# Optimization experiments

Hardware: AMD Instinct MI355X
Metric: run time of the kernel (lower is better)

## Reference

```python
import jax, jax.numpy as jnp
import numpy as np

B, T, D, H = 64, 512, 512, 512


def lstm_scan(x_btd, Wk, Wr, b):
    """Run an LSTM over time. x_btd: [B,T,D]. Returns (h_seq [B,T,H], h_last, c_last).
    Keras gate order: i, f, c(g), o."""
    Bsz = x_btd.shape[0]
    Hn = Wr.shape[0]
    # Precompute input projections for all timesteps in one GEMM: [B,T,4H]
    xz = jnp.einsum('btd,dg->btg', x_btd, Wk) + b

    def step(carry, xz_t):
        h, c = carry
        z = xz_t + h @ Wr  # [B,4H]
        i, f, g, o = jnp.split(z, 4, axis=-1)
        i = jax.nn.sigmoid(i)
        f = jax.nn.sigmoid(f)
        g = jnp.tanh(g)
        o = jax.nn.sigmoid(o)
        c = f * c + i * g
        h = o * jnp.tanh(c)
        return (h, c), h

    h0 = jnp.zeros((Bsz, Hn), dtype=x_btd.dtype)
    c0 = jnp.zeros((Bsz, Hn), dtype=x_btd.dtype)
    (h_last, c_last), h_seq = jax.lax.scan(step, (h0, c0), jnp.swapaxes(xz, 0, 1))
    return jnp.swapaxes(h_seq, 0, 1), h_last, c_last


def setup_inputs() -> dict:
    key = jax.random.key(0)
    ks = jax.random.split(key, 6)
    s_in = 1.0 / np.sqrt(D)
    s_h = 1.0 / np.sqrt(H)
    return {
        'x': jax.random.normal(ks[0], (B, T, D), dtype=jnp.float32),
        'Wf_k': jax.random.normal(ks[1], (D, 4 * H), dtype=jnp.float32) * s_in,
        'Wf_r': jax.random.normal(ks[2], (H, 4 * H), dtype=jnp.float32) * s_h,
        'bf': jnp.zeros((4 * H,), dtype=jnp.float32),
        'Wb_k': jax.random.normal(ks[3], (D, 4 * H), dtype=jnp.float32) * s_in,
        'Wb_r': jax.random.normal(ks[4], (H, 4 * H), dtype=jnp.float32) * s_h,
        'bb': jnp.zeros((4 * H,), dtype=jnp.float32),
    }


def reference(x, Wf_k, Wf_r, bf, Wb_k, Wb_r, bb):
    # Forward direction
    h_fwd_seq, h_fwd, _c_fwd = lstm_scan(x, Wf_k, Wf_r, bf)
    # Backward direction: run on time-reversed input, then flip outputs back
    x_rev = jnp.flip(x, axis=1)
    h_bwd_seq_rev, h_bwd, _c_bwd = lstm_scan(x_rev, Wb_k, Wb_r, bb)
    h_bwd_seq = jnp.flip(h_bwd_seq_rev, axis=1)
    # Bidirectional merge_mode='concat'
    word_emb = jnp.concatenate([h_fwd_seq, h_bwd_seq], axis=-1)  # [B,T,2H]
    sent_emb = jnp.concatenate([h_fwd, h_bwd], axis=-1)          # [B,2H]
    return (word_emb, sent_emb)
```

## Files before the change

### kernel.cpp

```cpp
#include <hip/hip_runtime.h>
#include <hip/hip_bf16.h>
#include <cstdint>
#include <cstddef>

#define Bsz 64
#define Tn  512
#define Dn  512
#define Hn  512
#define NG  2048
#define GWG 32
#define NCOL 16

typedef __attribute__((ext_vector_type(8))) short short8;
typedef __attribute__((ext_vector_type(4))) float f32x4;

union FragU { uint32_t u[4]; short8 s; };

__device__ __forceinline__ unsigned short f2bf(float f) {
  union { float f; uint32_t u; } v; v.f = f;
  uint32_t u = v.u;
  uint32_t r = (u + 0x7fffu + ((u >> 16) & 1u)) >> 16;
  return (unsigned short)r;
}

__device__ __forceinline__ float sigm(float x) { return 1.0f / (1.0f + __expf(-x)); }
__device__ __forceinline__ float tanh_f(float x) { return 1.0f - 2.0f / (__expf(2.0f * x) + 1.0f); }

__global__ __launch_bounds__(256) void cast_x_kernel(const float* __restrict__ x,
                                                     unsigned short* __restrict__ xb) {
  size_t i = ((size_t)blockIdx.x * 256 + threadIdx.x) * 8;
  f32x4 a = *(const f32x4*)(x + i);
  f32x4 b = *(const f32x4*)(x + i + 4);
  short8 r;
  r[0] = (short)f2bf(a[0]); r[1] = (short)f2bf(a[1]);
  r[2] = (short)f2bf(a[2]); r[3] = (short)f2bf(a[3]);
  r[4] = (short)f2bf(b[0]); r[5] = (short)f2bf(b[1]);
  r[6] = (short)f2bf(b[2]); r[7] = (short)f2bf(b[3]);
  *(short8*)(xb + i) = r;
}

__global__ __launch_bounds__(256) void swizzle_w_kernel(
    const float* __restrict__ Wfk, const float* __restrict__ Wfr,
    const float* __restrict__ Wbk, const float* __restrict__ Wbr,
    unsigned short* __restrict__ wkf, unsigned short* __restrict__ wrf)
{
  int idx = blockIdx.x * 256 + threadIdx.x;
  int arr  = blockIdx.y;
  int lane = idx & 63;
  int kc   = (idx >> 6) & 15;
  int nt   = (idx >> 10) & 3;
  int wg   = (idx >> 12) & 31;
  int dir  = (idx >> 17) & 1;
  const float* W = arr ? (dir ? Wbr : Wfr) : (dir ? Wbk : Wfk);
  unsigned short* dst = (arr ? wrf : wkf) + (size_t)idx * 8;
  int n  = nt * 512 + wg * NCOL + (lane & 15);
  int k0 = kc * 32 + ((lane >> 4) & 3) * 8;
#pragma unroll
  for (int j = 0; j < 8; ++j) dst[j] = f2bf(W[(size_t)(k0 + j) * NG + n]);
}

__global__ __launch_bounds__(256, 1) void lstm_main_kernel(
    const unsigned short* __restrict__ xb,
    const unsigned short* __restrict__ wkf,
    const unsigned short* __restrict__ wrf,
    const float* __restrict__ bias_f, const float* __restrict__ bias_b,
    unsigned short* __restrict__ hbuf,
    int* __restrict__ flags,
    float* __restrict__ out)
{
  const int wg   = blockIdx.x;
  const int dir  = blockIdx.y;
  const int tid  = threadIdx.x;
  const int lane = tid & 63;
  const int wv   = tid >> 6;
  const int quad = lane >> 4;
  const int col  = lane & 15;

  __shared__ short8 wr_lds[4 * 16 * 64];

  {
    const short8* src = (const short8*)wrf + (size_t)(dir * GWG + wg) * 4096;
    for (int i = tid; i < 4096; i += 256) wr_lds[i] = src[i];
  }
  const short8* wk = (const short8*)wkf + (size_t)(dir * GWG + wg) * 4096;

  const float* bias = dir ? bias_b : bias_f;
  float bz[4];
#pragma unroll
  for (int g = 0; g < 4; ++g) bz[g] = bias[g * 512 + wg * NCOL + col];

  float cst[4] = {0.f, 0.f, 0.f, 0.f};

  const int am = wv * 16 + col;
  unsigned short* hf_base = hbuf + (size_t)dir * 65536;
  int* flgbase = flags + dir * Tn * 4 * GWG;

  const int kcW = wg >> 1;
  const int c0  = col & ~1;
  const int qd2 = (((wg & 1) << 4) + c0) >> 3;
  const int j2  = c0 & 7;
  const int r0  = (col & 1) << 1;
  const int eBase = (((wv * 16 + kcW) * 64 + qd2 * 16 + quad * 4 + r0) * 8 + j2) >> 1;

  __syncthreads();

  for (int t = 0; t < Tn; ++t) {
    const int tx = dir ? (Tn - 1 - t) : t;
    f32x4 a0 = {0.f,0.f,0.f,0.f}, a1 = {0.f,0.f,0.f,0.f};
    f32x4 a2 = {0.f,0.f,0.f,0.f}, a3 = {0.f,0.f,0.f,0.f};

    const short8* xrow = (const short8*)(xb + ((size_t)am * Tn + tx) * Dn);
#pragma unroll 4
    for (int kc = 0; kc < 16; ++kc) {
      short8 a = xrow[kc * 4 + quad];
      a0 = __builtin_amdgcn_mfma_f32_16x16x32_bf16(a, wk[(0*16+kc)*64 + lane], a0, 0,0,0);
      a1 = __builtin_amdgcn_mfma_f32_16x16x32_bf16(a, wk[(1*16+kc)*64 + lane], a1, 0,0,0);
      a2 = __builtin_amdgcn_mfma_f32_16x16x32_bf16(a, wk[(2*16+kc)*64 + lane], a2, 0,0,0);
      a3 = __builtin_amdgcn_mfma_f32_16x16x32_bf16(a, wk[(3*16+kc)*64 + lane], a3, 0,0,0);
    }

    if (t > 0) {
      const int* fl = flgbase + ((t - 1) * 4 + wv) * GWG;
      for (;;) {
        int v = __hip_atomic_load(fl + (lane & 31), __ATOMIC_RELAXED, __HIP_MEMORY_SCOPE_AGENT);
        if (__ballot(v != 0) == ~0ull) break;
        __builtin_amdgcn_s_sleep(1);
      }
    }

    const uint32_t* hp = (const uint32_t*)(hf_base + ((t & 1) ^ 1) * 32768);
    uint32_t*       hc = (uint32_t*)(hf_base + (t & 1) * 32768);

    FragU hfr[16];
#pragma unroll
    for (int kc = 0; kc < 16; ++kc) {
      const uint32_t* p = hp + ((size_t)(wv * 16 + kc) * 64 + lane) * 4;
#pragma unroll
      for (int d = 0; d < 4; ++d)
        hfr[kc].u[d] = __hip_atomic_load(p + d, __ATOMIC_RELAXED, __HIP_MEMORY_SCOPE_AGENT);
    }

#pragma unroll
    for (int kc = 0; kc < 16; ++kc) {
      short8 a = hfr[kc].s;
      a0 = __builtin_amdgcn_mfma_f32_16x16x32_bf16(a, wr_lds[(0*16+kc)*64 + lane], a0, 0,0,0);
      a1 = __builtin_amdgcn_mfma_f32_16x16x32_bf16(a, wr_lds[(1*16+kc)*64 + lane], a1, 0,0,0);
      a2 = __builtin_amdgcn_mfma_f32_16x16x32_bf16(a, wr_lds[(2*16+kc)*64 + lane], a2, 0,0,0);
      a3 = __builtin_amdgcn_mfma_f32_16x16x32_bf16(a, wr_lds[(3*16+kc)*64 + lane], a3, 0,0,0);
    }

    float hv[4];
#pragma unroll
    for (int r = 0; r < 4; ++r) {
      float zi = a0[r] + bz[0];
      float zf = a1[r] + bz[1];
      float zg = a2[r] + bz[2];
      float zo = a3[r] + bz[3];
      float ig = sigm(zi);
      float fg = sigm(zf);
      float gg = tanh_f(zg);
      float og = sigm(zo);
      float c  = fg * cst[r] + ig * gg;
      cst[r] = c;
      hv[r] = og * tanh_f(c);
    }

    unsigned short hb16[4];
#pragma unroll
    for (int r = 0; r < 4; ++r) hb16[r] = f2bf(hv[r]);
    uint32_t msg = (col & 1) ? ((uint32_t)hb16[0] | ((uint32_t)hb16[1] << 16))
                             : ((uint32_t)hb16[2] | ((uint32_t)hb16[3] << 16));
    uint32_t got = (uint32_t)__shfl_xor((int)msg, 1);
    uint32_t pkA, pkB;
    if ((col & 1) == 0) {
      pkA = (uint32_t)hb16[0] | ((got & 0xffffu) << 16);
      pkB = (uint32_t)hb16[1] | ((got >> 16) << 16);
    } else {
      pkA = (got & 0xffffu) | ((uint32_t)hb16[2] << 16);
      pkB = (got >> 16)     | ((uint32_t)hb16[3] << 16);
    }
    __hip_atomic_store(hc + eBase,     pkA, __ATOMIC_RELAXED, __HIP_MEMORY_SCOPE_AGENT);
    __hip_atomic_store(hc + eBase + 4, pkB, __ATOMIC_RELAXED, __HIP_MEMORY_SCOPE_AGENT);

    __threadfence_block();
    __builtin_amdgcn_s_waitcnt(0);
    if (lane == 0)
      __hip_atomic_store(flgbase + (t * 4 + wv) * GWG + wg, 1,
                         __ATOMIC_RELAXED, __HIP_MEMORY_SCOPE_AGENT);

#pragma unroll
    for (int r = 0; r < 4; ++r) {
      const int b = wv * 16 + quad * 4 + r;
      out[((size_t)b * Tn + tx) * (2 * Hn) + dir * Hn + wg * NCOL + col] = hv[r];
      if (t == Tn - 1)
        out[(size_t)Bsz * Tn * (2 * Hn) + (size_t)b * (2 * Hn) + dir * Hn + wg * NCOL + col] = hv[r];
    }
  }
}

extern "C" void kernel_launch(void* const* d_in, const int* in_sizes, int n_in,
                              void* d_out, int out_size, void* d_ws, size_t ws_size,
                              hipStream_t stream) {
  const float* x   = (const float*)d_in[0];
  const float* Wfk = (const float*)d_in[1];
  const float* Wfr = (const float*)d_in[2];
  const float* bf_ = (const float*)d_in[3];
  const float* Wbk = (const float*)d_in[4];
  const float* Wbr = (const float*)d_in[5];
  const float* bb_ = (const float*)d_in[6];
  float* out = (float*)d_out;

  char* ws = (char*)d_ws;
  unsigned short* xb   = (unsigned short*)(ws);
  unsigned short* wkf  = (unsigned short*)(ws + 33554432);
  unsigned short* wrf  = (unsigned short*)(ws + 37748736);
  unsigned short* hbuf = (unsigned short*)(ws + 41943040);
  int*            flg  = (int*)           (ws + 42205184);

  hipMemsetAsync(ws + 41943040, 0, 262144 + 524288, stream);
  cast_x_kernel<<<8192, 256, 0, stream>>>(x, xb);
  swizzle_w_kernel<<<dim3(1024, 2), 256, 0, stream>>>(Wfk, Wfr, Wbk, Wbr, wkf, wrf);
  lstm_main_kernel<<<dim3(GWG, 2), 256, 0, stream>>>(xb, wkf, wrf, bf_, bb_, hbuf, flg, out);
}
```

Baseline: 4.907 ms.

## Replace flag barrier with sentinel-polled 8-slot h ring, cache Wk in LDS

Drops the per-step flag array and its wait loop. The hidden-state buffer becomes an 8-slot ring seeded with a sentinel value. Each step issues cache-bypassing loads of h, spins until no sentinel remains, and writers re-poison a future slot. This removes one round trip through memory (flag store, then flag poll, then data load) on the serial critical path. It also keeps the input-projection weights in 64 KB of extra LDS and prefetches the next timestep's x row into registers. The risks are correctness if a genuine bf16 pair ever equals the sentinel, and higher register and LDS pressure.

```diff
diff --git a/kernel.cpp b/kernel.cpp
--- a/kernel.cpp
+++ b/kernel.cpp
@@ -1,5 +1,4 @@
 #include <hip/hip_runtime.h>
-#include <hip/hip_bf16.h>
 #include <cstdint>
 #include <cstddef>
 
@@ -10,11 +9,13 @@
 #define NG  2048
 #define GWG 32
 #define NCOL 16
+#define SENTI 0x7f7f7f7fu
 
 typedef __attribute__((ext_vector_type(8))) short short8;
 typedef __attribute__((ext_vector_type(4))) float f32x4;
-
-union FragU { uint32_t u[4]; short8 s; };
+typedef __attribute__((ext_vector_type(4))) unsigned int u32x4;
+
+union FragU { u32x4 v; short8 s; };
 
 __device__ __forceinline__ unsigned short f2bf(float f) {
   union { float f; uint32_t u; } v; v.f = f;
@@ -65,7 +66,6 @@
     const unsigned short* __restrict__ wrf,
     const float* __restrict__ bias_f, const float* __restrict__ bias_b,
     unsigned short* __restrict__ hbuf,
-    int* __restrict__ flags,
     float* __restrict__ out)
 {
   const int wg   = blockIdx.x;
@@ -76,13 +76,15 @@
   const int quad = lane >> 4;
   const int col  = lane & 15;
 
-  __shared__ short8 wr_lds[4 * 16 * 64];
+  extern __shared__ char smem[];
+  short8* wr_lds = (short8*)smem;
+  short8* wk_lds = (short8*)(smem + 65536);
 
   {
-    const short8* src = (const short8*)wrf + (size_t)(dir * GWG + wg) * 4096;
-    for (int i = tid; i < 4096; i += 256) wr_lds[i] = src[i];
+    const short8* srcR = (const short8*)wrf + (size_t)(dir * GWG + wg) * 4096;
+    const short8* srcK = (const short8*)wkf + (size_t)(dir * GWG + wg) * 4096;
+    for (int i = tid; i < 4096; i += 256) { wr_lds[i] = srcR[i]; wk_lds[i] = srcK[i]; }
   }
-  const short8* wk = (const short8*)wkf + (size_t)(dir * GWG + wg) * 4096;
 
   const float* bias = dir ? bias_b : bias_f;
   float bz[4];
@@ -92,8 +94,7 @@
   float cst[4] = {0.f, 0.f, 0.f, 0.f};
 
   const int am = wv * 16 + col;
-  unsigned short* hf_base = hbuf + (size_t)dir * 65536;
-  int* flgbase = flags + dir * Tn * 4 * GWG;
+  unsigned short* ring = hbuf + (size_t)dir * (8 * 32768);
 
   const int kcW = wg >> 1;
   const int c0  = col & ~1;
@@ -102,42 +103,71 @@
   const int r0  = (col & 1) << 1;
   const int eBase = (((wv * 16 + kcW) * 64 + qd2 * 16 + quad * 4 + r0) * 8 + j2) >> 1;
 
+  short8 xr[16];
+  {
+    const int tx0 = dir ? (Tn - 1) : 0;
+    const short8* xrow = (const short8*)(xb + ((size_t)am * Tn + tx0) * Dn);
+#pragma unroll
+    for (int kc = 0; kc < 16; ++kc) xr[kc] = xrow[kc * 4 + quad];
+  }
+
   __syncthreads();
+
+#define HL(idx, base, offs) \
+  asm volatile("global_load_dwordx4 %0, %1, off" offs " sc0 sc1" \
+               : "=v"(hfr[idx].v) : "v"(base))
+#define HISSUE() do { \
+    const char* b0_ = hb; const char* b1_ = hb + 4096; \
+    const char* b2_ = hb + 8192; const char* b3_ = hb + 12288; \
+    HL(0,  b0_, "");               HL(1,  b0_, " offset:1024"); \
+    HL(2,  b0_, " offset:2048");   HL(3,  b0_, " offset:3072"); \
+    HL(4,  b1_, "");               HL(5,  b1_, " offset:1024"); \
+    HL(6,  b1_, " offset:2048");   HL(7,  b1_, " offset:3072"); \
+    HL(8,  b2_, "");               HL(9,  b2_, " offset:1024"); \
+    HL(10, b2_, " offset:2048");   HL(11, b2_, " offset:3072"); \
+    HL(12, b3_, "");               HL(13, b3_, " offset:1024"); \
+    HL(14, b3_, " offset:2048");   HL(15, b3_, " offset:3072"); \
+  } while (0)
 
   for (int t = 0; t < Tn; ++t) {
     const int tx = dir ? (Tn - 1 - t) : t;
     f32x4 a0 = {0.f,0.f,0.f,0.f}, a1 = {0.f,0.f,0.f,0.f};
     f32x4 a2 = {0.f,0.f,0.f,0.f}, a3 = {0.f,0.f,0.f,0.f};
 
-    const short8* xrow = (const short8*)(xb + ((size_t)am * Tn + tx) * Dn);
+    FragU hfr[16];
+    const char* hb = (const char*)ring + (size_t)(t & 7) * 65536
+                   + ((size_t)(wv * 16) * 64 + lane) * 16;
+    HISSUE();
+
 #pragma unroll 4
     for (int kc = 0; kc < 16; ++kc) {
-      short8 a = xrow[kc * 4 + quad];
-      a0 = __builtin_amdgcn_mfma_f32_16x16x32_bf16(a, wk[(0*16+kc)*64 + lane], a0, 0,0,0);
-      a1 = __builtin_amdgcn_mfma_f32_16x16x32_bf16(a, wk[(1*16+kc)*64 + lane], a1, 0,0,0);
-      a2 = __builtin_amdgcn_mfma_f32_16x16x32_bf16(a, wk[(2*16+kc)*64 + lane], a2, 0,0,0);
-      a3 = __builtin_amdgcn_mfma_f32_16x16x32_bf16(a, wk[(3*16+kc)*64 + lane], a3, 0,0,0);
-    }
-
-    if (t > 0) {
-      const int* fl = flgbase + ((t - 1) * 4 + wv) * GWG;
-      for (;;) {
-        int v = __hip_atomic_load(fl + (lane & 31), __ATOMIC_RELAXED, __HIP_MEMORY_SCOPE_AGENT);
-        if (__ballot(v != 0) == ~0ull) break;
-        __builtin_amdgcn_s_sleep(1);
+      short8 a = xr[kc];
+      a0 = __builtin_amdgcn_mfma_f32_16x16x32_bf16(a, wk_lds[(0*16+kc)*64 + lane], a0, 0,0,0);
+      a1 = __builtin_amdgcn_mfma_f32_16x16x32_bf16(a, wk_lds[(1*16+kc)*64 + lane], a1, 0,0,0);
+      a2 = __builtin_amdgcn_mfma_f32_16x16x32_bf16(a, wk_lds[(2*16+kc)*64 + lane], a2, 0,0,0);
+      a3 = __builtin_amdgcn_mfma_f32_16x16x32_bf16(a, wk_lds[(3*16+kc)*64 + lane], a3, 0,0,0);
+    }
+
+    if (t < Tn - 1) {
+      const int txn = dir ? (Tn - 2 - t) : (t + 1);
+      const short8* xrow = (const short8*)(xb + ((size_t)am * Tn + txn) * Dn);
+#pragma unroll
+      for (int kc = 0; kc < 16; ++kc) xr[kc] = xrow[kc * 4 + quad];
+    }
+
+    for (;;) {
+      asm volatile("s_waitcnt vmcnt(0)" ::: "memory");
+      __builtin_amdgcn_sched_barrier(0);
+      int ok = 1;
+#pragma unroll
+      for (int kc = 0; kc < 16; ++kc) {
+        ok &= (hfr[kc].v[0] != SENTI);
+        ok &= (hfr[kc].v[1] != SENTI);
+        ok &= (hfr[kc].v[2] != SENTI);
+        ok &= (hfr[kc].v[3] != SENTI);
       }
-    }
-
-    const uint32_t* hp = (const uint32_t*)(hf_base + ((t & 1) ^ 1) * 32768);
-    uint32_t*       hc = (uint32_t*)(hf_base + (t & 1) * 32768);
-
-    FragU hfr[16];
-#pragma unroll
-    for (int kc = 0; kc < 16; ++kc) {
-      const uint32_t* p = hp + ((size_t)(wv * 16 + kc) * 64 + lane) * 4;
-#pragma unroll
-      for (int d = 0; d < 4; ++d)
-        hfr[kc].u[d] = __hip_atomic_load(p + d, __ATOMIC_RELAXED, __HIP_MEMORY_SCOPE_AGENT);
+      if (__ballot(!ok) == 0ull) break;
+      HISSUE();
     }
 
 #pragma unroll
@@ -179,14 +209,12 @@
       pkA = (got & 0xffffu) | ((uint32_t)hb16[2] << 16);
       pkB = (got >> 16)     | ((uint32_t)hb16[3] << 16);
     }
+    uint32_t* hc = (uint32_t*)((char*)ring + (size_t)((t + 1) & 7) * 65536);
+    uint32_t* hx = (uint32_t*)((char*)ring + (size_t)((t + 5) & 7) * 65536);
     __hip_atomic_store(hc + eBase,     pkA, __ATOMIC_RELAXED, __HIP_MEMORY_SCOPE_AGENT);
     __hip_atomic_store(hc + eBase + 4, pkB, __ATOMIC_RELAXED, __HIP_MEMORY_SCOPE_AGENT);
-
-    __threadfence_block();
-    __builtin_amdgcn_s_waitcnt(0);
-    if (lane == 0)
-      __hip_atomic_store(flgbase + (t * 4 + wv) * GWG + wg, 1,
-                         __ATOMIC_RELAXED, __HIP_MEMORY_SCOPE_AGENT);
+    __hip_atomic_store(hx + eBase,     SENTI, __ATOMIC_RELAXED, __HIP_MEMORY_SCOPE_AGENT);
+    __hip_atomic_store(hx + eBase + 4, SENTI, __ATOMIC_RELAXED, __HIP_MEMORY_SCOPE_AGENT);
 
 #pragma unroll
     for (int r = 0; r < 4; ++r) {
@@ -196,6 +224,8 @@
         out[(size_t)Bsz * Tn * (2 * Hn) + (size_t)b * (2 * Hn) + dir * Hn + wg * NCOL + col] = hv[r];
     }
   }
+#undef HISSUE
+#undef HL
 }
 
 extern "C" void kernel_launch(void* const* d_in, const int* in_sizes, int n_in,
@@ -215,10 +245,15 @@
   unsigned short* wkf  = (unsigned short*)(ws + 33554432);
   unsigned short* wrf  = (unsigned short*)(ws + 37748736);
   unsigned short* hbuf = (unsigned short*)(ws + 41943040);
-  int*            flg  = (int*)           (ws + 42205184);
-
-  hipMemsetAsync(ws + 41943040, 0, 262144 + 524288, stream);
+
+  hipMemsetAsync(ws + 41943040, 0x7f, 1048576, stream);
+  hipMemsetAsync(ws + 41943040, 0x00, 65536, stream);
+  hipMemsetAsync(ws + 41943040 + 524288, 0x00, 65536, stream);
+
   cast_x_kernel<<<8192, 256, 0, stream>>>(x, xb);
   swizzle_w_kernel<<<dim3(1024, 2), 256, 0, stream>>>(Wfk, Wfr, Wbk, Wbr, wkf, wrf);
-  lstm_main_kernel<<<dim3(GWG, 2), 256, 0, stream>>>(xb, wkf, wrf, bf_, bb_, hbuf, flg, out);
-}
+
+  (void)hipFuncSetAttribute((const void*)lstm_main_kernel,
+                            hipFuncAttributeMaxDynamicSharedMemorySize, 131072);
+  lstm_main_kernel<<<dim3(GWG, 2), 256, 131072, stream>>>(xb, wkf, wrf, bf_, bb_, hbuf, out);
+}
```

Result: slower. 6.272 ms (+27.8%).
